# Kernel tuning notes

Measured on AMD Instinct MI355X. Metric: run time of the kernel, lower is better.

## Reference

```python
import jax, jax.numpy as jnp
import numpy as np

N = 50000      # nodes
E = 800000     # edges
D_IN, D_H, D_OUT = 256, 256, 128
BN_EPS = 1e-5


def setup_inputs() -> dict:
    key = jax.random.key(0)
    ks = jax.random.split(key, 16)
    inp = {}
    inp["x"] = jax.random.normal(ks[0], (N, D_IN), dtype=jnp.float32)
    inp["edge_index"] = jax.random.randint(ks[1], (2, E), 0, N, dtype=jnp.int32)
    s1 = 1.0 / np.sqrt(D_IN)
    s2 = 1.0 / np.sqrt(D_H)
    inp["W1"] = jax.random.normal(ks[2], (D_IN, D_H), dtype=jnp.float32) * s1
    inp["b1"] = jnp.zeros((D_H,), dtype=jnp.float32)
    inp["g1"] = jnp.ones((D_H,), dtype=jnp.float32)
    inp["be1"] = jnp.zeros((D_H,), dtype=jnp.float32)
    inp["m1"] = jax.random.normal(ks[3], (D_H,), dtype=jnp.float32) * 0.1
    inp["v1"] = jax.random.uniform(ks[4], (D_H,), dtype=jnp.float32, minval=0.5, maxval=1.5)
    inp["W2"] = jax.random.normal(ks[5], (D_H, D_H), dtype=jnp.float32) * s2
    inp["b2"] = jnp.zeros((D_H,), dtype=jnp.float32)
    inp["g2"] = jnp.ones((D_H,), dtype=jnp.float32)
    inp["be2"] = jnp.zeros((D_H,), dtype=jnp.float32)
    inp["m2"] = jax.random.normal(ks[6], (D_H,), dtype=jnp.float32) * 0.1
    inp["v2"] = jax.random.uniform(ks[7], (D_H,), dtype=jnp.float32, minval=0.5, maxval=1.5)
    inp["W3"] = jax.random.normal(ks[8], (D_H, D_OUT), dtype=jnp.float32) * s2
    inp["b3"] = jnp.zeros((D_OUT,), dtype=jnp.float32)
    return inp


def reference(x, edge_index, W1, b1, g1, be1, m1, v1,
              W2, b2, g2, be2, m2, v2, W3, b3):
    # Add self-loops (PyG GCNConv default) and compute symmetric normalization once.
    loop = jnp.arange(N, dtype=edge_index.dtype)
    src = jnp.concatenate([edge_index[0], loop])   # [E+N]
    dst = jnp.concatenate([edge_index[1], loop])   # [E+N]
    deg = jax.ops.segment_sum(jnp.ones_like(dst, dtype=x.dtype), dst, num_segments=N)
    dinv = jax.lax.rsqrt(deg)                      # deg >= 1 thanks to self-loops
    norm = (dinv[src] * dinv[dst])[:, None]        # [E+N, 1]

    def gcn_conv(h, W, b):
        h = h @ W                                   # [N, D]
        agg = jax.ops.segment_sum(h[src] * norm, dst, num_segments=N)
        return agg + b

    def bn_eval(h, g, be, m, v):
        return (h - m) * (g * jax.lax.rsqrt(v + BN_EPS)) + be

    h = jax.nn.relu(bn_eval(gcn_conv(x, W1, b1), g1, be1, m1, v1))  # dropout = identity (eval)
    h = jax.nn.relu(bn_eval(gcn_conv(h, W2, b2), g2, be2, m2, v2))
    out = gcn_conv(h, W3, b3)                       # [N, D_OUT]
    return out
```

## Files before the change

### kernel.cpp

```cpp
#include <hip/hip_runtime.h>
#include <hip/hip_bf16.h>
#include <hip/hip_fp16.h>


#define GN 50000
#define GE 800000

typedef float f32x4 __attribute__((ext_vector_type(4)));
typedef _Float16 f16x8 __attribute__((ext_vector_type(8)));


__global__ __launch_bounds__(256) void init_kernel(int* counts, int* cursor, int* total) {
    int i = blockIdx.x * 256 + threadIdx.x;
    if (i < GN) { counts[i] = 0; cursor[i] = 0; }
    if (i == 0) *total = 0;
}

__global__ __launch_bounds__(256) void count_kernel(const int* __restrict__ dst, int* __restrict__ counts) {
    int e = blockIdx.x * 256 + threadIdx.x;
    if (e < GE) atomicAdd(&counts[dst[e]], 1);
}

__global__ __launch_bounds__(256) void alloc_kernel(const int* __restrict__ counts, float* __restrict__ dinv,
                                                    int* __restrict__ base, int* __restrict__ total) {
    int i = blockIdx.x * 256 + threadIdx.x;
    int lane = threadIdx.x & 63;
    int c = (i < GN) ? counts[i] : 0;
    if (i < GN) dinv[i] = rsqrtf((float)c + 1.0f);
    int v = c;
#pragma unroll
    for (int off = 1; off < 64; off <<= 1) {
        int t = __shfl_up(v, off);
        if (lane >= off) v += t;
    }
    int waveSum = __shfl(v, 63);
    int wb = 0;
    if (lane == 63) wb = atomicAdd(total, waveSum);
    wb = __shfl(wb, 63);
    if (i < GN) base[i] = wb + v - c;
}

__global__ __launch_bounds__(256) void fill_kernel(const int* __restrict__ src, const int* __restrict__ dst,
                                                   const int* __restrict__ base, int* __restrict__ cursor,
                                                   int* __restrict__ col) {
    int e = blockIdx.x * 256 + threadIdx.x;
    if (e < GE) {
        int d = dst[e];
        int pos = base[d] + atomicAdd(&cursor[d], 1);
        col[pos] = src[e];
    }
}

__global__ __launch_bounds__(256) void params_kernel(
    const float* b1, const float* g1, const float* be1, const float* m1, const float* v1,
    const float* b2, const float* g2, const float* be2, const float* m2, const float* v2,
    float* prm) {
    int t = threadIdx.x;
    float s1 = g1[t] * rsqrtf(v1[t] + 1e-5f);
    prm[0 * 256 + t] = s1;
    prm[1 * 256 + t] = (b1[t] - m1[t]) * s1 + be1[t];
    float s2 = g2[t] * rsqrtf(v2[t] + 1e-5f);
    prm[2 * 256 + t] = s2;
    prm[3 * 256 + t] = (b2[t] - m2[t]) * s2 + be2[t];
}


__global__ __launch_bounds__(256) void conv_x(const float* __restrict__ in, ushort* __restrict__ out, int n4) {
    int i = blockIdx.x * 256 + threadIdx.x;
    if (i >= n4) return;
    float4 v = *(const float4*)&in[(size_t)i * 4];
    ushort4 h;
    h.x = __half_as_ushort(__float2half_rn(v.x));
    h.y = __half_as_ushort(__float2half_rn(v.y));
    h.z = __half_as_ushort(__float2half_rn(v.z));
    h.w = __half_as_ushort(__float2half_rn(v.w));
    *(ushort4*)&out[(size_t)i * 4] = h;
}

__global__ __launch_bounds__(256) void transpose_all(const float* __restrict__ W1, const float* __restrict__ W2,
                                                     const float* __restrict__ W3,
                                                     ushort* __restrict__ T1, ushort* __restrict__ T2,
                                                     ushort* __restrict__ T3) {
    int idx = blockIdx.x * 256 + threadIdx.x;
    const float* W;
    ushort* T;
    int i, DO;
    if (idx < 65536) { W = W1; T = T1; i = idx; DO = 256; }
    else if (idx < 131072) { W = W2; T = T2; i = idx - 65536; DO = 256; }
    else if (idx < 163840) { W = W3; T = T3; i = idx - 131072; DO = 128; }
    else return;
    int n = i >> 8, k = i & 255;
    T[i] = __half_as_ushort(__float2half_rn(W[k * DO + n]));
}


template <int DO>
__global__ __launch_bounds__(256) void gemm_mfma(const ushort* __restrict__ A16, const ushort* __restrict__ B16,
                                                 const float* __restrict__ dinv, __half* __restrict__ C, int M) {
    __shared__ ushort lds[2][128][40];
    int tid = threadIdx.x;
    int lane = tid & 63;
    int wave = tid >> 6;
    int wm = wave >> 1, wn = wave & 1;
    int m0 = blockIdx.x * 128;
    int n0 = blockIdx.y * 128;
    int rsel = lane & 15;
    int ksel = (lane >> 4) * 8;

    int o0 = tid * 16, o1 = (tid + 256) * 16;
    int row0 = o0 >> 6, kb0 = o0 & 63;
    int row1 = o1 >> 6, kb1 = o1 & 63;
    int rA0 = min(m0 + row0, M - 1), rA1 = min(m0 + row1, M - 1);
    int rB0 = min(n0 + row0, DO - 1), rB1 = min(n0 + row1, DO - 1);

    uint4 vA0, vA1, vB0, vB1;
    auto loadregs = [&](int k0) {
        const char* a = (const char*)A16;
        const char* b = (const char*)B16;
        vA0 = *(const uint4*)(a + (size_t)rA0 * 512 + (size_t)k0 * 2 + kb0);
        vA1 = *(const uint4*)(a + (size_t)rA1 * 512 + (size_t)k0 * 2 + kb1);
        vB0 = *(const uint4*)(b + (size_t)rB0 * 512 + (size_t)k0 * 2 + kb0);
        vB1 = *(const uint4*)(b + (size_t)rB1 * 512 + (size_t)k0 * 2 + kb1);
    };
    auto writelds = [&]() {
        *(uint4*)((char*)&lds[0][row0][0] + kb0) = vA0;
        *(uint4*)((char*)&lds[0][row1][0] + kb1) = vA1;
        *(uint4*)((char*)&lds[1][row0][0] + kb0) = vB0;
        *(uint4*)((char*)&lds[1][row1][0] + kb1) = vB1;
    };

    f32x4 acc[4][4] = {};

    loadregs(0);
    for (int k0 = 0; k0 < 256; k0 += 32) {
        writelds();
        __syncthreads();
        if (k0 + 32 < 256) loadregs(k0 + 32);

        f16x8 bv[4];
#pragma unroll
        for (int ni = 0; ni < 4; ni++)
            bv[ni] = *(const f16x8*)&lds[1][wn * 64 + ni * 16 + rsel][ksel];
#pragma unroll
        for (int mi = 0; mi < 4; mi++) {
            f16x8 av = *(const f16x8*)&lds[0][wm * 64 + mi * 16 + rsel][ksel];
#pragma unroll
            for (int ni = 0; ni < 4; ni++)
                acc[mi][ni] = __builtin_amdgcn_mfma_f32_16x16x32_f16(av, bv[ni], acc[mi][ni], 0, 0, 0);
        }
        __syncthreads();
    }

#pragma unroll
    for (int mi = 0; mi < 4; mi++) {
#pragma unroll
        for (int j = 0; j < 4; j++) {
            int r = m0 + wm * 64 + mi * 16 + (lane >> 4) * 4 + j;
            if (r < M) {
                float dv = dinv[r];
#pragma unroll
                for (int ni = 0; ni < 4; ni++) {
                    int c = n0 + wn * 64 + ni * 16 + rsel;
                    C[(size_t)r * DO + c] = __float2half_rn(acc[mi][ni][j] * dv);
                }
            }
        }
    }
}

template <int D, int MODE>
__global__ __launch_bounds__(256) void agg_kernel(const __half* __restrict__ Hs, const int* __restrict__ base,
                                                  const int* __restrict__ counts, const float* __restrict__ dinv,
                                                  const int* __restrict__ col,
                                                  const float* __restrict__ pa, const float* __restrict__ pc,
                                                  float* __restrict__ outF, ushort* __restrict__ outH, int M) {
    constexpr int V = D / 64;
    constexpr int P = V / 2;
    int w = blockIdx.x * 4 + (threadIdx.x >> 6);
    if (w >= M) return;
    int lane = threadIdx.x & 63;
    const char* gbase = (const char*)(Hs + lane * V);
    float2 acc2[P];
#pragma unroll
    for (int j = 0; j < P; j++) acc2[j] = make_float2(0.f, 0.f);

    auto accum32 = [&](unsigned bits, int j2) {
        __half2 h = *(__half2*)&bits;
        float2 f = __half22float2(h);
        acc2[j2].x += f.x;
        acc2[j2].y += f.y;
    };

    if constexpr (V == 4) {
        uint2 r = *(const uint2*)(gbase + (size_t)w * D * 2);
        accum32(r.x, 0); accum32(r.y, 1);
    } else {
        unsigned r = *(const unsigned*)(gbase + (size_t)w * D * 2);
        accum32(r, 0);
    }

    int e = base[w], end = e + counts[w];
    for (; e + 8 <= end; e += 8) {
        int idx[8];
#pragma unroll
        for (int t = 0; t < 8; t++) idx[t] = col[e + t];
        if constexpr (V == 4) {
            uint2 r[8];
#pragma unroll
            for (int t = 0; t < 8; t++) r[t] = *(const uint2*)(gbase + (size_t)idx[t] * (D * 2));
#pragma unroll
            for (int t = 0; t < 8; t++) { accum32(r[t].x, 0); accum32(r[t].y, 1); }
        } else {
            unsigned r[8];
#pragma unroll
            for (int t = 0; t < 8; t++) r[t] = *(const unsigned*)(gbase + (size_t)idx[t] * (D * 2));
#pragma unroll
            for (int t = 0; t < 8; t++) accum32(r[t], 0);
        }
    }
    for (; e < end; e++) {
        int s = col[e];
        if constexpr (V == 4) {
            uint2 r = *(const uint2*)(gbase + (size_t)s * (D * 2));
            accum32(r.x, 0); accum32(r.y, 1);
        } else {
            unsigned r = *(const unsigned*)(gbase + (size_t)s * (D * 2));
            accum32(r, 0);
        }
    }

    float dv = dinv[w];
    float acc[V];
#pragma unroll
    for (int j = 0; j < P; j++) { acc[2 * j] = acc2[j].x; acc[2 * j + 1] = acc2[j].y; }

    if constexpr (MODE == 1) {
        ushort4 h;
        int d = lane * V;
        float val;
        val = fmaxf(fmaf(acc[0] * dv, pa[d + 0], pc[d + 0]), 0.f);
        h.x = __half_as_ushort(__float2half_rn(val));
        val = fmaxf(fmaf(acc[1] * dv, pa[d + 1], pc[d + 1]), 0.f);
        h.y = __half_as_ushort(__float2half_rn(val));
        val = fmaxf(fmaf(acc[2] * dv, pa[d + 2], pc[d + 2]), 0.f);
        h.z = __half_as_ushort(__float2half_rn(val));
        val = fmaxf(fmaf(acc[3] * dv, pa[d + 3], pc[d + 3]), 0.f);
        h.w = __half_as_ushort(__float2half_rn(val));
        *(ushort4*)&outH[(size_t)w * D + d] = h;
    } else {
#pragma unroll
        for (int j = 0; j < V; j++) {
            int d = lane * V + j;
            outF[(size_t)w * D + d] = acc[j] * dv + pa[d];
        }
    }
}


extern "C" void kernel_launch(void* const* d_in, const int* in_sizes, int n_in,
                              void* d_out, int out_size, void* d_ws, size_t ws_size,
                              hipStream_t stream) {
    const float* x = (const float*)d_in[0];
    const int* ei = (const int*)d_in[1];
    const int* srcIdx = ei;
    const int* dstIdx = ei + GE;
    const float* W1 = (const float*)d_in[2];
    const float* b1 = (const float*)d_in[3];
    const float* g1 = (const float*)d_in[4];
    const float* be1 = (const float*)d_in[5];
    const float* m1 = (const float*)d_in[6];
    const float* v1 = (const float*)d_in[7];
    const float* W2 = (const float*)d_in[8];
    const float* b2 = (const float*)d_in[9];
    const float* g2 = (const float*)d_in[10];
    const float* be2 = (const float*)d_in[11];
    const float* m2 = (const float*)d_in[12];
    const float* v2 = (const float*)d_in[13];
    const float* W3 = (const float*)d_in[14];
    const float* b3 = (const float*)d_in[15];
    float* out = (float*)d_out;

    size_t off = 0;
    char* wsb = (char*)d_ws;
    auto take = [&](size_t bytes) -> char* {
        char* p = wsb + off;
        off += (bytes + 255) & ~(size_t)255;
        return p;
    };
    float* dinv = (float*)take((size_t)GN * 4);
    int* counts = (int*)take((size_t)GN * 4);
    int* cursor = (int*)take((size_t)GN * 4);
    int* segbase = (int*)take((size_t)GN * 4);
    int* total = (int*)take(256);
    int* col = (int*)take((size_t)GE * 4);
    float* prm = (float*)take(4 * 256 * 4);
    __half* hH = (__half*)take((size_t)GN * 256 * 2);
    ushort* P = (ushort*)take((size_t)GN * 256 * 2);
    ushort* X16 = P;
    ushort* WT1 = (ushort*)take(256 * 256 * 2);
    ushort* WT2 = (ushort*)take(256 * 256 * 2);
    ushort* WT3 = (ushort*)take(128 * 256 * 2);

    const float* a1 = prm + 0 * 256;
    const float* c1 = prm + 1 * 256;
    const float* a2 = prm + 2 * 256;
    const float* c2 = prm + 3 * 256;

    int nb = (GN + 255) / 256;
    int eb = (GE + 255) / 256;

    init_kernel<<<nb, 256, 0, stream>>>(counts, cursor, total);
    count_kernel<<<eb, 256, 0, stream>>>(dstIdx, counts);
    alloc_kernel<<<nb, 256, 0, stream>>>(counts, dinv, segbase, total);
    fill_kernel<<<eb, 256, 0, stream>>>(srcIdx, dstIdx, segbase, cursor, col);
    params_kernel<<<1, 256, 0, stream>>>(b1, g1, be1, m1, v1, b2, g2, be2, m2, v2, prm);

    int n4 = GN * 64;
    conv_x<<<(n4 + 255) / 256, 256, 0, stream>>>(x, X16, n4);
    transpose_all<<<(163840 + 255) / 256, 256, 0, stream>>>(W1, W2, W3, WT1, WT2, WT3);

    dim3 gg((GN + 127) / 128, 2);
    dim3 gg3((GN + 127) / 128, 1);
    int ab = (GN + 3) / 4;

    gemm_mfma<256><<<gg, 256, 0, stream>>>(X16, WT1, dinv, hH, GN);
    agg_kernel<256, 1><<<ab, 256, 0, stream>>>(hH, segbase, counts, dinv, col, a1, c1, nullptr, P, GN);
    gemm_mfma<256><<<gg, 256, 0, stream>>>(P, WT2, dinv, hH, GN);
    agg_kernel<256, 1><<<ab, 256, 0, stream>>>(hH, segbase, counts, dinv, col, a2, c2, nullptr, P, GN);
    gemm_mfma<128><<<gg3, 256, 0, stream>>>(P, WT3, dinv, hH, GN);
    agg_kernel<128, 0><<<ab, 256, 0, stream>>>(hH, segbase, counts, dinv, col, b3, b3, out, nullptr, GN);
}
```

Baseline: 440.7 us.

## Fuse fp32-to-fp16 input conversion into GEMM and cover full N per block

Removes the separate conv_x kernel and lets the first GEMM read fp32 x directly, converting to fp16 while staging into LDS. The 256-wide GEMMs now use 512-thread blocks that compute all output columns, so each A tile is loaded once instead of twice across two grid columns. This cuts a full pass over x (write and re-read of fp16 copy) and halves A traffic, at the cost of larger blocks, more registers and doubled fp32 load bytes in the first GEMM.

```diff
diff --git a/kernel.cpp b/kernel.cpp
--- a/kernel.cpp
+++ b/kernel.cpp
@@ -62,19 +62,6 @@
     float s2 = g2[t] * rsqrtf(v2[t] + 1e-5f);
     prm[2 * 256 + t] = s2;
     prm[3 * 256 + t] = (b2[t] - m2[t]) * s2 + be2[t];
-}
-
-
-__global__ __launch_bounds__(256) void conv_x(const float* __restrict__ in, ushort* __restrict__ out, int n4) {
-    int i = blockIdx.x * 256 + threadIdx.x;
-    if (i >= n4) return;
-    float4 v = *(const float4*)&in[(size_t)i * 4];
-    ushort4 h;
-    h.x = __half_as_ushort(__float2half_rn(v.x));
-    h.y = __half_as_ushort(__float2half_rn(v.y));
-    h.z = __half_as_ushort(__float2half_rn(v.z));
-    h.w = __half_as_ushort(__float2half_rn(v.w));
-    *(ushort4*)&out[(size_t)i * 4] = h;
 }
 
 __global__ __launch_bounds__(256) void transpose_all(const float* __restrict__ W1, const float* __restrict__ W2,
@@ -94,39 +81,75 @@
 }
 
 
-template <int DO>
-__global__ __launch_bounds__(256) void gemm_mfma(const ushort* __restrict__ A16, const ushort* __restrict__ B16,
-                                                 const float* __restrict__ dinv, __half* __restrict__ C, int M) {
-    __shared__ ushort lds[2][128][40];
+template <int DO, bool AF32>
+__global__ __launch_bounds__((DO == 256) ? 512 : 256) void gemm_mfma(
+    const void* __restrict__ Ap, const ushort* __restrict__ B16,
+    const float* __restrict__ dinv, __half* __restrict__ C, int M) {
+    constexpr int THREADS = (DO == 256) ? 512 : 256;
+    constexpr int WN = DO / 64;
+    constexpr int AC = 8192 / 16 / THREADS;
+    constexpr int BC = DO * 64 / 16 / THREADS;
+
+    __shared__ ushort ldsA[128][40];
+    __shared__ ushort ldsB[DO][40];
+
     int tid = threadIdx.x;
     int lane = tid & 63;
     int wave = tid >> 6;
-    int wm = wave >> 1, wn = wave & 1;
+    int wm = wave / WN, wn = wave % WN;
     int m0 = blockIdx.x * 128;
-    int n0 = blockIdx.y * 128;
     int rsel = lane & 15;
     int ksel = (lane >> 4) * 8;
 
-    int o0 = tid * 16, o1 = (tid + 256) * 16;
-    int row0 = o0 >> 6, kb0 = o0 & 63;
-    int row1 = o1 >> 6, kb1 = o1 & 63;
-    int rA0 = min(m0 + row0, M - 1), rA1 = min(m0 + row1, M - 1);
-    int rB0 = min(n0 + row0, DO - 1), rB1 = min(n0 + row1, DO - 1);
-
-    uint4 vA0, vA1, vB0, vB1;
+    int aRow[AC], aKb[AC], aGr[AC];
+#pragma unroll
+    for (int c = 0; c < AC; c++) {
+        int o = (tid + c * THREADS) * 16;
+        aRow[c] = o >> 6; aKb[c] = o & 63;
+        aGr[c] = min(m0 + aRow[c], M - 1);
+    }
+    int bRow[BC], bKb[BC];
+#pragma unroll
+    for (int c = 0; c < BC; c++) {
+        int o = (tid + c * THREADS) * 16;
+        bRow[c] = o >> 6; bKb[c] = o & 63;
+    }
+
+    uint4 hA[AC];
+    float4 fA[AC][2];
+    uint4 hB[BC];
     auto loadregs = [&](int k0) {
-        const char* a = (const char*)A16;
-        const char* b = (const char*)B16;
-        vA0 = *(const uint4*)(a + (size_t)rA0 * 512 + (size_t)k0 * 2 + kb0);
-        vA1 = *(const uint4*)(a + (size_t)rA1 * 512 + (size_t)k0 * 2 + kb1);
-        vB0 = *(const uint4*)(b + (size_t)rB0 * 512 + (size_t)k0 * 2 + kb0);
-        vB1 = *(const uint4*)(b + (size_t)rB1 * 512 + (size_t)k0 * 2 + kb1);
+#pragma unroll
+        for (int c = 0; c < AC; c++) {
+            if constexpr (AF32) {
+                const char* a = (const char*)Ap;
+                fA[c][0] = *(const float4*)(a + (size_t)aGr[c] * 1024 + (size_t)k0 * 4 + aKb[c] * 2);
+                fA[c][1] = *(const float4*)(a + (size_t)aGr[c] * 1024 + (size_t)k0 * 4 + aKb[c] * 2 + 16);
+            } else {
+                const char* a = (const char*)Ap;
+                hA[c] = *(const uint4*)(a + (size_t)aGr[c] * 512 + (size_t)k0 * 2 + aKb[c]);
+            }
+        }
+#pragma unroll
+        for (int c = 0; c < BC; c++)
+            hB[c] = *(const uint4*)((const char*)B16 + (size_t)bRow[c] * 512 + (size_t)k0 * 2 + bKb[c]);
+    };
+    auto p2 = [](float x, float y) -> unsigned {
+        return ((unsigned)__half_as_ushort(__float2half_rn(y)) << 16) | __half_as_ushort(__float2half_rn(x));
     };
     auto writelds = [&]() {
-        *(uint4*)((char*)&lds[0][row0][0] + kb0) = vA0;
-        *(uint4*)((char*)&lds[0][row1][0] + kb1) = vA1;
-        *(uint4*)((char*)&lds[1][row0][0] + kb0) = vB0;
-        *(uint4*)((char*)&lds[1][row1][0] + kb1) = vB1;
+#pragma unroll
+        for (int c = 0; c < AC; c++) {
+            uint4 v;
+            if constexpr (AF32) {
+                v.x = p2(fA[c][0].x, fA[c][0].y); v.y = p2(fA[c][0].z, fA[c][0].w);
+                v.z = p2(fA[c][1].x, fA[c][1].y); v.w = p2(fA[c][1].z, fA[c][1].w);
+            } else v = hA[c];
+            *(uint4*)((char*)&ldsA[aRow[c]][0] + aKb[c]) = v;
+        }
+#pragma unroll
+        for (int c = 0; c < BC; c++)
+            *(uint4*)((char*)&ldsB[bRow[c]][0] + bKb[c]) = hB[c];
     };
 
     f32x4 acc[4][4] = {};
@@ -140,10 +163,10 @@
         f16x8 bv[4];
 #pragma unroll
         for (int ni = 0; ni < 4; ni++)
-            bv[ni] = *(const f16x8*)&lds[1][wn * 64 + ni * 16 + rsel][ksel];
+            bv[ni] = *(const f16x8*)&ldsB[wn * 64 + ni * 16 + rsel][ksel];
 #pragma unroll
         for (int mi = 0; mi < 4; mi++) {
-            f16x8 av = *(const f16x8*)&lds[0][wm * 64 + mi * 16 + rsel][ksel];
+            f16x8 av = *(const f16x8*)&ldsA[wm * 64 + mi * 16 + rsel][ksel];
 #pragma unroll
             for (int ni = 0; ni < 4; ni++)
                 acc[mi][ni] = __builtin_amdgcn_mfma_f32_16x16x32_f16(av, bv[ni], acc[mi][ni], 0, 0, 0);
@@ -160,7 +183,7 @@
                 float dv = dinv[r];
 #pragma unroll
                 for (int ni = 0; ni < 4; ni++) {
-                    int c = n0 + wn * 64 + ni * 16 + rsel;
+                    int c = wn * 64 + ni * 16 + rsel;
                     C[(size_t)r * DO + c] = __float2half_rn(acc[mi][ni][j] * dv);
                 }
             }
@@ -296,7 +319,6 @@
     float* prm = (float*)take(4 * 256 * 4);
     __half* hH = (__half*)take((size_t)GN * 256 * 2);
     ushort* P = (ushort*)take((size_t)GN * 256 * 2);
-    ushort* X16 = P;
     ushort* WT1 = (ushort*)take(256 * 256 * 2);
     ushort* WT2 = (ushort*)take(256 * 256 * 2);
     ushort* WT3 = (ushort*)take(128 * 256 * 2);
@@ -314,19 +336,15 @@
     alloc_kernel<<<nb, 256, 0, stream>>>(counts, dinv, segbase, total);
     fill_kernel<<<eb, 256, 0, stream>>>(srcIdx, dstIdx, segbase, cursor, col);
     params_kernel<<<1, 256, 0, stream>>>(b1, g1, be1, m1, v1, b2, g2, be2, m2, v2, prm);
-
-    int n4 = GN * 64;
-    conv_x<<<(n4 + 255) / 256, 256, 0, stream>>>(x, X16, n4);
     transpose_all<<<(163840 + 255) / 256, 256, 0, stream>>>(W1, W2, W3, WT1, WT2, WT3);
 
-    dim3 gg((GN + 127) / 128, 2);
-    dim3 gg3((GN + 127) / 128, 1);
+    int gblocks = (GN + 127) / 128;
     int ab = (GN + 3) / 4;
 
-    gemm_mfma<256><<<gg, 256, 0, stream>>>(X16, WT1, dinv, hH, GN);
+    gemm_mfma<256, true><<<gblocks, 512, 0, stream>>>(x, WT1, dinv, hH, GN);
     agg_kernel<256, 1><<<ab, 256, 0, stream>>>(hH, segbase, counts, dinv, col, a1, c1, nullptr, P, GN);
-    gemm_mfma<256><<<gg, 256, 0, stream>>>(P, WT2, dinv, hH, GN);
+    gemm_mfma<256, false><<<gblocks, 512, 0, stream>>>(P, WT2, dinv, hH, GN);
     agg_kernel<256, 1><<<ab, 256, 0, stream>>>(hH, segbase, counts, dinv, col, a2, c2, nullptr, P, GN);
-    gemm_mfma<128><<<gg3, 256, 0, stream>>>(P, WT3, dinv, hH, GN);
+    gemm_mfma<128, false><<<gblocks, 256, 0, stream>>>(P, WT3, dinv, hH, GN);
     agg_kernel<128, 0><<<ab, 256, 0, stream>>>(hH, segbase, counts, dinv, col, b3, b3, out, nullptr, GN);
 }
```

After: 463.4 us. 5.2% more time.
